# Optimization experiments

Measured on AMD Instinct MI355X. Metric: run time of the kernel, lower is better.

The kernel has to match this reference:

```python
import jax, jax.numpy as jnp
import numpy as np

S_MUL, V_MUL = 32, 16          # 32x0e + 16x1o
NODE_DIM = S_MUL + 3 * V_MUL   # 80
LATENT = 128
INV_SQRT3 = 1.0 / np.sqrt(3.0)          # wigner 3j (1,1,0) / (0,1,1) / (1,0,1) factor
C_SCALAR = np.float32(1.0 / np.sqrt(48.0))   # path_norm 'element': fan into 0e = 32*1 + 16*1
C_VECTOR = np.float32(np.sqrt(3.0 / 48.0))   # irrep dim 3 / fan 48 for 1o output


def setup_inputs() -> dict:
    rng = np.random.default_rng(0)
    B, n_atoms, radius = 2048, 32, 5.0
    N = B * n_atoms
    # atoms uniform in a 10A cube -> ~300 edges per 32-atom graph at r=5
    pos_g = rng.uniform(0.0, 10.0, size=(B, n_atoms, 3)).astype(np.float32)
    diff = pos_g[:, :, None, :] - pos_g[:, None, :, :]
    d2 = (diff * diff).sum(-1)
    mask = (d2 <= radius * radius) & (d2 > 0.0)   # same predicate as build_radius_graph
    b_idx, i_idx, j_idx = np.nonzero(mask)
    edge_index = np.stack([b_idx * n_atoms + i_idx, b_idx * n_atoms + j_idx]).astype(np.int32)
    pos = pos_g.reshape(N, 3)
    z = rng.integers(0, 100, size=N).astype(np.int32)
    batch = np.repeat(np.arange(B, dtype=np.int32), n_atoms)
    L = 3  # num_layers

    def w(*shape, scale=1.0):
        return jnp.asarray((rng.standard_normal(shape) * scale).astype(np.float32))

    return dict(
        pos=jnp.asarray(pos), z=jnp.asarray(z), batch=jnp.asarray(batch),
        edge_index=jnp.asarray(edge_index), num_graphs=B,
        emb=w(100, S_MUL),                      # nn.Embedding(100, 32) ~ N(0,1)
        W_s2n=w(S_MUL, S_MUL),                  # e3nn Linear 32x0e -> 32x0e path
        W1=w(L, S_MUL, S_MUL),                  # tp path 0e x 0e -> 0e
        W2=w(L, S_MUL, V_MUL),                  # tp path 0e x 1o -> 1o
        W3=w(L, V_MUL, V_MUL),                  # tp path 1o x 0e -> 1o
        W4=w(L, V_MUL, S_MUL),                  # tp path 1o x 1o -> 0e
        Ws=w(L, S_MUL, S_MUL),                  # e3nn Linear scalar block
        Wv=w(L, V_MUL, V_MUL),                  # e3nn Linear vector block
        Wr1=w(NODE_DIM, 256, scale=1.0 / np.sqrt(NODE_DIM)), br1=jnp.zeros((256,), jnp.float32),
        Wr2=w(256, LATENT, scale=1.0 / np.sqrt(256.0)), br2=jnp.zeros((LATENT,), jnp.float32),
    )


def _forward(pos, emb, W_s2n, W1, W2, W3, W4, Ws, Wv, Wr1, br1, Wr2, br2,
             z, batch, edge_index, num_graphs):
    N = pos.shape[0]
    src, dst = edge_index[0], edge_index[1]
    # atom embedding -> node irreps (only 0e->0e path exists; vectors start at 0)
    s = (emb[z] @ W_s2n) * np.float32(1.0 / np.sqrt(S_MUL))   # (N, 32)
    v = jnp.zeros((N, V_MUL, 3), pos.dtype)                   # (N, 16, 3)
    # spherical harmonics, normalize=True, 'component': Y0 = 1, Y1 = sqrt(3) * r_hat
    rij = pos[dst] - pos[src]                                 # (E, 3)
    sh1 = np.float32(np.sqrt(3.0)) * rij / jnp.linalg.norm(rij, axis=-1, keepdims=True)
    for l in range(W1.shape[0]):
        ss, vs = s[src], v[src]                               # gather (E,32), (E,16,3)
        # FullyConnectedTensorProduct(node, sh, node), uvw weights, sh0 == 1
        m_s = C_SCALAR * (jnp.einsum('eu,uw->ew', ss, W1[l])
                          + INV_SQRT3 * jnp.einsum('eui,ei,uw->ew', vs, sh1, W4[l]))
        m_v = (C_VECTOR * INV_SQRT3) * (jnp.einsum('eu,ei,uw->ewi', ss, sh1, W2[l])
                                        + jnp.einsum('eui,uw->ewi', vs, W3[l]))
        a_s = jax.ops.segment_sum(m_s, dst, num_segments=N)   # index_add_ scatter
        a_v = jax.ops.segment_sum(m_v, dst, num_segments=N)
        # e3nn Linear (per-irrep block, 1/sqrt(fan_in)) then relu on FULL feature (as in source)
        h_s = jax.nn.relu((a_s @ Ws[l]) * np.float32(1.0 / np.sqrt(S_MUL)))
        h_v = jax.nn.relu(jnp.einsum('nvi,vw->nwi', a_v, Wv[l]) * np.float32(1.0 / np.sqrt(V_MUL)))
        s, v = s + h_s, v + h_v                               # residual
    x = jnp.concatenate([s, v.reshape(N, V_MUL * 3)], axis=-1)  # (N, 80)
    hg = jax.ops.segment_sum(x, batch, num_segments=num_graphs) # sum-pool per graph
    return jax.nn.relu(hg @ Wr1 + br1) @ Wr2 + br2              # (B, latent)


def reference(pos, emb, W_s2n, W1, W2, W3, W4, Ws, Wv, Wr1, br1, Wr2, br2,
              z, batch, edge_index, num_graphs):
    return _forward(pos, emb, W_s2n, W1, W2, W3, W4, Ws, Wv, Wr1, br1, Wr2, br2,
                    z, batch, edge_index, num_graphs)
```

## Files before the change

kernel.cpp:

```cpp
#include <hip/hip_runtime.h>
#include <math.h>

typedef __attribute__((ext_vector_type(8))) short bf16x8;
typedef __attribute__((ext_vector_type(4))) float f32x4;

#define SQRT3F     1.7320508075688772f
#define SCALE_T    0.17677669529663687f
#define SCALE_M1   0.025515518153991442f
#define SCALE_M2   0.014731391274719739f
#define SCALE_M34  0.036084391824351615f

#define FSTR 40
#define ASTR 72

__device__ __forceinline__ ushort f2bf(float f) {
    union { float f; unsigned u; } v; v.f = f;
    unsigned u = v.u;
    return (ushort)((u + 0x7FFFu + ((u >> 16) & 1u)) >> 16);
}
__device__ __forceinline__ float bf2f(ushort h) {
    union { unsigned u; float f; } v; v.u = ((unsigned)h) << 16;
    return v.f;
}
__device__ __forceinline__ unsigned cvtpk(float lo, float hi) {
    unsigned r;
    asm("v_cvt_pk_bf16_f32 %0, %1, %2" : "=v"(r) : "v"(lo), "v"(hi));
    return r;
}
__device__ __forceinline__ f32x4 mfma(bf16x8 a, bf16x8 b, f32x4 c) {
    return __builtin_amdgcn_mfma_f32_16x16x32_bf16(a, b, c, 0, 0, 0);
}
__device__ __forceinline__ void storeAgg(ushort* AG, f32x4 t, int u0, int n) {
    uint2 u;
    u.x = cvtpk(t[0], t[1]);
    u.y = cvtpk(t[2], t[3]);
    *(uint2*)&AG[n*ASTR + u0] = u;
}
__device__ __forceinline__ void rmw4(ushort* F, int c, int n0, f32x4 h) {
    uint2* p = (uint2*)&F[c*FSTR + n0];
    uint2 o = *p;
    float f0 = bf2f((ushort)(o.x      )) + fmaxf(h[0], 0.f);
    float f1 = bf2f((ushort)(o.x >> 16)) + fmaxf(h[1], 0.f);
    float f2 = bf2f((ushort)(o.y      )) + fmaxf(h[2], 0.f);
    float f3 = bf2f((ushort)(o.y >> 16)) + fmaxf(h[3], 0.f);
    uint2 w;
    w.x = cvtpk(f0, f1);
    w.y = cvtpk(f2, f3);
    *p = w;
}

__global__ void prep_kernel(const float* __restrict__ emb,
                            const float* __restrict__ W_s2n,
                            const float* __restrict__ W1, const float* __restrict__ W2,
                            const float* __restrict__ W3, const float* __restrict__ W4,
                            const float* __restrict__ Ws, const float* __restrict__ Wv,
                            ushort* __restrict__ Tbf, ushort* __restrict__ Mbf)
{
    int idx = blockIdx.x * blockDim.x + threadIdx.x;
    if (idx < 3200) {
        int r = idx >> 5, c = idx & 31;
        float acc = 0.f;
        for (int k = 0; k < 32; ++k) acc += emb[r*32 + k] * W_s2n[k*32 + c];
        Tbf[idx] = f2bf(acc * SCALE_T);
        return;
    }
    idx -= 3200;
    if (idx < 3*48*64) {
        int lyr = idx / 3072, rem = idx % 3072;
        int row = rem >> 6, u = rem & 63;
        float val = 0.f;
        if (row < 32) {
            int w = row;
            if (u < 32) {
                float a = 0.f;
                for (int k = 0; k < 32; ++k)
                    a += W1[lyr*1024 + u*32 + k] * Ws[lyr*1024 + k*32 + w];
                val = a * SCALE_M1;
            } else if (u < 48) {
                int uu = u - 32; float a = 0.f;
                for (int k = 0; k < 32; ++k)
                    a += W4[lyr*512 + uu*32 + k] * Ws[lyr*1024 + k*32 + w];
                val = a * SCALE_M2;
            }
        } else {
            int w = row - 32;
            if (u < 32) {
                float a = 0.f;
                for (int k = 0; k < 16; ++k)
                    a += W2[lyr*512 + u*16 + k] * Wv[lyr*256 + k*16 + w];
                val = a * SCALE_M34;
            } else if (u < 48) {
                int uu = u - 32; float a = 0.f;
                for (int k = 0; k < 16; ++k)
                    a += W3[lyr*256 + uu*16 + k] * Wv[lyr*256 + k*16 + w];
                val = a * SCALE_M34;
            }
        }
        Mbf[lyr*3072 + row*64 + u] = f2bf(val);
    }
}

__global__ __launch_bounds__(256)
void gnn_kernel(const float* __restrict__ pos, const int* __restrict__ z,
                const ushort* __restrict__ Tbf, const ushort* __restrict__ Mbf,
                const float* __restrict__ Wr1, const float* __restrict__ br1,
                const float* __restrict__ Wr2, const float* __restrict__ br2,
                float* __restrict__ out, int B)
{
    __shared__ __align__(16) char smem[45312];
    ushort* featA = (ushort*)smem;
    ushort* aggA  = (ushort*)(smem + 25600);
    float*  hgl   = (float*)(smem + 44032);
    float*  h1    = (float*)aggA;
    float*  red   = ((float*)aggA) + 1024;

    const int tid = threadIdx.x;
    const int wv = tid >> 6, l = tid & 63;
    const int g  = blockIdx.x*4 + wv;
    ushort* F  = featA + wv*80*FSTR;
    ushort* AG = aggA  + wv*32*ASTR;

    for (int i = l; i < 32*(ASTR/2); i += 64) ((uint*)AG)[i] = 0;
    for (int i = l; i < 48*(FSTR/2); i += 64) ((uint*)(F + 32*FSTR))[i] = 0;

    {
        int n = l & 31, h = l >> 5;
        int zg = z[g*32 + n];
        uint4 t0 = *(const uint4*)(Tbf + zg*32 + h*16);
        uint4 t1 = *(const uint4*)(Tbf + zg*32 + h*16 + 8);
        unsigned ua[8] = {t0.x, t0.y, t0.z, t0.w, t1.x, t1.y, t1.z, t1.w};
        #pragma unroll
        for (int q = 0; q < 8; ++q) {
            F[(h*16 + 2*q    )*FSTR + n] = (ushort)ua[q];
            F[(h*16 + 2*q + 1)*FSTR + n] = (ushort)(ua[q] >> 16);
        }
    }

    const int ln = l & 15, kq = l >> 4;
    bf16x8 adjf[4][2];
    {
        const int k0 = kq*8;
        #pragma unroll
        for (int nt = 0; nt < 2; ++nt) {
            int ng = g*32 + nt*16 + ln;
            float px = pos[3*ng], py = pos[3*ng+1], pz = pos[3*ng+2];
            union { bf16x8 v; ushort s[8]; } o[4];
            #pragma unroll
            for (int jj = 0; jj < 8; ++jj) {
                int j = g*32 + k0 + jj;
                float dx = __fsub_rn(px, pos[3*j]);
                float dy = __fsub_rn(py, pos[3*j+1]);
                float dz = __fsub_rn(pz, pos[3*j+2]);
                float d2 = __fadd_rn(__fadd_rn(__fmul_rn(dx,dx), __fmul_rn(dy,dy)),
                                     __fmul_rn(dz,dz));
                bool on = (d2 <= 25.0f) && (d2 > 0.0f);
                float rinv = on ? rsqrtf(d2) * SQRT3F : 0.f;
                o[0].s[jj] = on ? (ushort)0x3F80 : (ushort)0;
                o[1].s[jj] = f2bf(dx * rinv);
                o[2].s[jj] = f2bf(dy * rinv);
                o[3].s[jj] = f2bf(dz * rinv);
            }
            #pragma unroll
            for (int w = 0; w < 4; ++w) adjf[w][nt] = o[w].v;
        }
    }

    const f32x4 z4 = {0.f, 0.f, 0.f, 0.f};

    for (int lay = 0; lay < 3; ++lay) {
        const ushort* Mg = Mbf + lay*3072;
        bf16x8 fs0 = *(const bf16x8*)&F[(     ln)*FSTR + kq*8];
        bf16x8 fs1 = *(const bf16x8*)&F[(16 + ln)*FSTR + kq*8];
        bf16x8 fv0 = *(const bf16x8*)&F[(32 + ln)*FSTR + kq*8];
        bf16x8 fv1 = *(const bf16x8*)&F[(48 + ln)*FSTR + kq*8];
        bf16x8 fv2 = *(const bf16x8*)&F[(64 + ln)*FSTR + kq*8];
        bf16x8 bmS0[2], bmS1[2], bmV[2];
        #pragma unroll
        for (int kc = 0; kc < 2; ++kc) {
            bmS0[kc] = *(const bf16x8*)&Mg[(     ln)*64 + kc*32 + kq*8];
            bmS1[kc] = *(const bf16x8*)&Mg[(16 + ln)*64 + kc*32 + kq*8];
            bmV [kc] = *(const bf16x8*)&Mg[(32 + ln)*64 + kc*32 + kq*8];
        }

        #pragma unroll
        for (int nt = 0; nt < 2; ++nt) {
            f32x4 t;
            t = mfma(fs0, adjf[0][nt], z4);
            storeAgg(AG, t,      kq*4, nt*16 + ln);
            t = mfma(fs1, adjf[0][nt], z4);
            storeAgg(AG, t, 16 + kq*4, nt*16 + ln);
            t = mfma(fv2, adjf[3][nt], z4);
            t = mfma(fv1, adjf[2][nt], t);
            t = mfma(fv0, adjf[1][nt], t);
            storeAgg(AG, t, 32 + kq*4, nt*16 + ln);
        }
        f32x4 hs[2][2] = {{z4, z4}, {z4, z4}};
        #pragma unroll
        for (int kc = 0; kc < 2; ++kc)
            #pragma unroll
            for (int mt = 0; mt < 2; ++mt) {
                bf16x8 ag = *(const bf16x8*)&AG[(mt*16 + ln)*ASTR + kc*32 + kq*8];
                hs[mt][0] = mfma(ag, bmS0[kc], hs[mt][0]);
                hs[mt][1] = mfma(ag, bmS1[kc], hs[mt][1]);
            }
        #pragma unroll
        for (int mt = 0; mt < 2; ++mt)
            #pragma unroll
            for (int wt = 0; wt < 2; ++wt)
                rmw4(F, wt*16 + ln, mt*16 + kq*4, hs[mt][wt]);

        #pragma unroll
        for (int i = 0; i < 3; ++i) {
            bf16x8 fvi = (i == 0) ? fv0 : (i == 1) ? fv1 : fv2;
            #pragma unroll
            for (int nt = 0; nt < 2; ++nt) {
                f32x4 t;
                t = mfma(fs0, adjf[1+i][nt], z4);
                storeAgg(AG, t,      kq*4, nt*16 + ln);
                t = mfma(fs1, adjf[1+i][nt], z4);
                storeAgg(AG, t, 16 + kq*4, nt*16 + ln);
                t = mfma(fvi, adjf[0][nt], z4);
                storeAgg(AG, t, 32 + kq*4, nt*16 + ln);
            }
            f32x4 hv[2] = {z4, z4};
            #pragma unroll
            for (int kc = 0; kc < 2; ++kc)
                #pragma unroll
                for (int mt = 0; mt < 2; ++mt) {
                    bf16x8 ag = *(const bf16x8*)&AG[(mt*16 + ln)*ASTR + kc*32 + kq*8];
                    hv[mt] = mfma(ag, bmV[kc], hv[mt]);
                }
            #pragma unroll
            for (int mt = 0; mt < 2; ++mt)
                rmw4(F, 32 + i*16 + ln, mt*16 + kq*4, hv[mt]);
        }
    }

    for (int f = l; f < 80; f += 64) {
        const ushort* row;
        if (f < 32) row = &F[f*FSTR];
        else { int c = f - 32, w = c/3, i = c - 3*w; row = &F[(32 + i*16 + w)*FSTR]; }
        const uint* r32 = (const uint*)row;
        float acc = 0.f;
        #pragma unroll
        for (int q = 0; q < 16; ++q) {
            uint u = r32[q];
            acc += bf2f((ushort)u) + bf2f((ushort)(u >> 16));
        }
        hgl[wv*80 + f] = acc;
    }
    __syncthreads();

    {
        const int w = tid;
        float acc0 = br1[w];
        float acc1 = acc0, acc2 = acc0, acc3 = acc0;
        #pragma unroll 4
        for (int f = 0; f < 80; ++f) {
            float wvv = Wr1[f*256 + w];
            acc0 = fmaf(hgl[0*80 + f], wvv, acc0);
            acc1 = fmaf(hgl[1*80 + f], wvv, acc1);
            acc2 = fmaf(hgl[2*80 + f], wvv, acc2);
            acc3 = fmaf(hgl[3*80 + f], wvv, acc3);
        }
        h1[0*256 + w] = fmaxf(acc0, 0.f);
        h1[1*256 + w] = fmaxf(acc1, 0.f);
        h1[2*256 + w] = fmaxf(acc2, 0.f);
        h1[3*256 + w] = fmaxf(acc3, 0.f);
    }
    __syncthreads();
    {
        const int g0 = blockIdx.x * 4;
        const int w2 = tid & 127, kh = tid >> 7;
        const float4* h1v = (const float4*)h1;
        float s0 = 0.f, s1 = 0.f, s2 = 0.f, s3 = 0.f;
        #pragma unroll 2
        for (int k4 = kh*32; k4 < kh*32 + 32; ++k4) {
            float4 hA = h1v[0*64 + k4];
            float4 hB = h1v[1*64 + k4];
            float4 hC = h1v[2*64 + k4];
            float4 hD = h1v[3*64 + k4];
            int k = k4 * 4;
            float m0 = Wr2[(size_t)(k+0)*128 + w2];
            float m1 = Wr2[(size_t)(k+1)*128 + w2];
            float m2 = Wr2[(size_t)(k+2)*128 + w2];
            float m3 = Wr2[(size_t)(k+3)*128 + w2];
            s0 = fmaf(hA.x,m0, fmaf(hA.y,m1, fmaf(hA.z,m2, fmaf(hA.w,m3, s0))));
            s1 = fmaf(hB.x,m0, fmaf(hB.y,m1, fmaf(hB.z,m2, fmaf(hB.w,m3, s1))));
            s2 = fmaf(hC.x,m0, fmaf(hC.y,m1, fmaf(hC.z,m2, fmaf(hC.w,m3, s2))));
            s3 = fmaf(hD.x,m0, fmaf(hD.y,m1, fmaf(hD.z,m2, fmaf(hD.w,m3, s3))));
        }
        if (kh) {
            red[0*128 + w2] = s0; red[1*128 + w2] = s1;
            red[2*128 + w2] = s2; red[3*128 + w2] = s3;
        }
        __syncthreads();
        if (!kh) {
            float b = br2[w2];
            out[(size_t)(g0+0)*128 + w2] = s0 + red[0*128 + w2] + b;
            out[(size_t)(g0+1)*128 + w2] = s1 + red[1*128 + w2] + b;
            out[(size_t)(g0+2)*128 + w2] = s2 + red[2*128 + w2] + b;
            out[(size_t)(g0+3)*128 + w2] = s3 + red[3*128 + w2] + b;
        }
    }
}

extern "C" void kernel_launch(void* const* d_in, const int* in_sizes, int n_in,
                              void* d_out, int out_size, void* d_ws, size_t ws_size,
                              hipStream_t stream)
{
    const float* pos   = (const float*)d_in[0];
    const int*   z     = (const int*)d_in[1];
    const float* emb   = (const float*)d_in[5];
    const float* W_s2n = (const float*)d_in[6];
    const float* W1    = (const float*)d_in[7];
    const float* W2    = (const float*)d_in[8];
    const float* W3    = (const float*)d_in[9];
    const float* W4    = (const float*)d_in[10];
    const float* Ws    = (const float*)d_in[11];
    const float* Wv    = (const float*)d_in[12];
    const float* Wr1   = (const float*)d_in[13];
    const float* br1   = (const float*)d_in[14];
    const float* Wr2   = (const float*)d_in[15];
    const float* br2   = (const float*)d_in[16];
    float* out = (float*)d_out;

    const int B = out_size / 128;

    char* p = (char*)d_ws;
    ushort* Tbf = (ushort*)p;  p += 6400;
    ushort* Mbf = (ushort*)p;  p += 18432;

    const int prep_total = 3200 + 3*48*64;
    prep_kernel<<<(prep_total + 255) / 256, 256, 0, stream>>>(
        emb, W_s2n, W1, W2, W3, W4, Ws, Wv, Tbf, Mbf);

    gnn_kernel<<<B / 4, 256, 0, stream>>>(pos, z, Tbf, Mbf,
                                          Wr1, br1, Wr2, br2, out, B);
}
```

Before: 113.8 us.

## Keep aggregation tiles in registers via permlane swaps instead of LDS

The aggregated MFMA outputs are now repacked directly into B-operand fragments with permlane32/permlane16 swaps, instead of being written to a shared-memory staging buffer and reloaded. This drops the LDS store/load round trip and cuts shared memory per block, which may allow more blocks per CU. In exchange it adds software bf16 rounding and cross-lane permute instructions, and the register-to-fragment layout has to be exactly right.

```diff
diff --git a/kernel.cpp b/kernel.cpp
--- a/kernel.cpp
+++ b/kernel.cpp
@@ -11,7 +11,6 @@
 #define SCALE_M34  0.036084391824351615f
 
 #define FSTR 40
-#define ASTR 72
 
 __device__ __forceinline__ ushort f2bf(float f) {
     union { float f; unsigned u; } v; v.f = f;
@@ -22,19 +21,38 @@
     union { unsigned u; float f; } v; v.u = ((unsigned)h) << 16;
     return v.f;
 }
+__device__ __forceinline__ unsigned packbf(float lo, float hi) {
+    return (unsigned)f2bf(lo) | ((unsigned)f2bf(hi) << 16);
+}
 __device__ __forceinline__ unsigned cvtpk(float lo, float hi) {
     unsigned r;
     asm("v_cvt_pk_bf16_f32 %0, %1, %2" : "=v"(r) : "v"(lo), "v"(hi));
     return r;
 }
+__device__ __forceinline__ void pl32(unsigned &a, unsigned &b) {
+    auto r = __builtin_amdgcn_permlane32_swap(a, b, false, false);
+    a = r[0]; b = r[1];
+}
+__device__ __forceinline__ void pl16(unsigned &a, unsigned &b) {
+    auto r = __builtin_amdgcn_permlane16_swap(a, b, false, false);
+    a = r[0]; b = r[1];
+}
 __device__ __forceinline__ f32x4 mfma(bf16x8 a, bf16x8 b, f32x4 c) {
     return __builtin_amdgcn_mfma_f32_16x16x32_bf16(a, b, c, 0, 0, 0);
 }
-__device__ __forceinline__ void storeAgg(ushort* AG, f32x4 t, int u0, int n) {
-    uint2 u;
-    u.x = cvtpk(t[0], t[1]);
-    u.y = cvtpk(t[2], t[3]);
-    *(uint2*)&AG[n*ASTR + u0] = u;
+__device__ __forceinline__ void makeFrags(f32x4 T0, f32x4 T1, f32x4 T2,
+                                          bf16x8 &f0, bf16x8 &f1) {
+    unsigned p0 = packbf(T0[0], T0[1]), p1 = packbf(T0[2], T0[3]);
+    unsigned q0 = packbf(T1[0], T1[1]), q1 = packbf(T1[2], T1[3]);
+    unsigned s0 = packbf(T2[0], T2[1]), s1 = packbf(T2[2], T2[3]);
+    pl32(p0, q0); pl16(p0, q0);
+    pl32(p1, q1); pl16(p1, q1);
+    unsigned z0 = 0u, z1 = 0u;
+    pl32(s0, z0); pl16(s0, z0);
+    pl32(s1, z1); pl16(s1, z1);
+    union { bf16x8 v; unsigned u[4]; } r;
+    r.u[0] = p0; r.u[1] = p1; r.u[2] = q0; r.u[3] = q1; f0 = r.v;
+    r.u[0] = s0; r.u[1] = s1; r.u[2] = z0; r.u[3] = z1; f1 = r.v;
 }
 __device__ __forceinline__ void rmw4(ushort* F, int c, int n0, f32x4 h) {
     uint2* p = (uint2*)&F[c*FSTR + n0];
@@ -107,20 +125,17 @@
                 const float* __restrict__ Wr2, const float* __restrict__ br2,
                 float* __restrict__ out, int B)
 {
-    __shared__ __align__(16) char smem[45312];
+    __shared__ __align__(16) char smem[26880];
     ushort* featA = (ushort*)smem;
-    ushort* aggA  = (ushort*)(smem + 25600);
-    float*  hgl   = (float*)(smem + 44032);
-    float*  h1    = (float*)aggA;
-    float*  red   = ((float*)aggA) + 1024;
+    float*  hgl   = (float*)(smem + 25600);
+    float*  h1    = (float*)smem;
+    float*  red   = (float*)(smem + 4096);
 
     const int tid = threadIdx.x;
     const int wv = tid >> 6, l = tid & 63;
     const int g  = blockIdx.x*4 + wv;
     ushort* F  = featA + wv*80*FSTR;
-    ushort* AG = aggA  + wv*32*ASTR;
-
-    for (int i = l; i < 32*(ASTR/2); i += 64) ((uint*)AG)[i] = 0;
+
     for (int i = l; i < 48*(FSTR/2); i += 64) ((uint*)(F + 32*FSTR))[i] = 0;
 
     {
@@ -182,26 +197,24 @@
             bmV [kc] = *(const bf16x8*)&Mg[(32 + ln)*64 + kc*32 + kq*8];
         }
 
+        bf16x8 agf[2][2];
+
         #pragma unroll
         for (int nt = 0; nt < 2; ++nt) {
-            f32x4 t;
-            t = mfma(fs0, adjf[0][nt], z4);
-            storeAgg(AG, t,      kq*4, nt*16 + ln);
-            t = mfma(fs1, adjf[0][nt], z4);
-            storeAgg(AG, t, 16 + kq*4, nt*16 + ln);
-            t = mfma(fv2, adjf[3][nt], z4);
-            t = mfma(fv1, adjf[2][nt], t);
-            t = mfma(fv0, adjf[1][nt], t);
-            storeAgg(AG, t, 32 + kq*4, nt*16 + ln);
+            f32x4 T0 = mfma(fs0, adjf[0][nt], z4);
+            f32x4 T1 = mfma(fs1, adjf[0][nt], z4);
+            f32x4 T2 = mfma(fv2, adjf[3][nt], z4);
+            T2 = mfma(fv1, adjf[2][nt], T2);
+            T2 = mfma(fv0, adjf[1][nt], T2);
+            makeFrags(T0, T1, T2, agf[nt][0], agf[nt][1]);
         }
         f32x4 hs[2][2] = {{z4, z4}, {z4, z4}};
         #pragma unroll
         for (int kc = 0; kc < 2; ++kc)
             #pragma unroll
             for (int mt = 0; mt < 2; ++mt) {
-                bf16x8 ag = *(const bf16x8*)&AG[(mt*16 + ln)*ASTR + kc*32 + kq*8];
-                hs[mt][0] = mfma(ag, bmS0[kc], hs[mt][0]);
-                hs[mt][1] = mfma(ag, bmS1[kc], hs[mt][1]);
+                hs[mt][0] = mfma(agf[mt][kc], bmS0[kc], hs[mt][0]);
+                hs[mt][1] = mfma(agf[mt][kc], bmS1[kc], hs[mt][1]);
             }
         #pragma unroll
         for (int mt = 0; mt < 2; ++mt)
@@ -214,22 +227,17 @@
             bf16x8 fvi = (i == 0) ? fv0 : (i == 1) ? fv1 : fv2;
             #pragma unroll
             for (int nt = 0; nt < 2; ++nt) {
-                f32x4 t;
-                t = mfma(fs0, adjf[1+i][nt], z4);
-                storeAgg(AG, t,      kq*4, nt*16 + ln);
-                t = mfma(fs1, adjf[1+i][nt], z4);
-                storeAgg(AG, t, 16 + kq*4, nt*16 + ln);
-                t = mfma(fvi, adjf[0][nt], z4);
-                storeAgg(AG, t, 32 + kq*4, nt*16 + ln);
+                f32x4 T0 = mfma(fs0, adjf[1+i][nt], z4);
+                f32x4 T1 = mfma(fs1, adjf[1+i][nt], z4);
+                f32x4 T2 = mfma(fvi, adjf[0][nt], z4);
+                makeFrags(T0, T1, T2, agf[nt][0], agf[nt][1]);
             }
             f32x4 hv[2] = {z4, z4};
             #pragma unroll
             for (int kc = 0; kc < 2; ++kc)
                 #pragma unroll
-                for (int mt = 0; mt < 2; ++mt) {
-                    bf16x8 ag = *(const bf16x8*)&AG[(mt*16 + ln)*ASTR + kc*32 + kq*8];
-                    hv[mt] = mfma(ag, bmV[kc], hv[mt]);
-                }
+                for (int mt = 0; mt < 2; ++mt)
+                    hv[mt] = mfma(agf[mt][kc], bmV[kc], hv[mt]);
             #pragma unroll
             for (int mt = 0; mt < 2; ++mt)
                 rmw4(F, 32 + i*16 + ln, mt*16 + kq*4, hv[mt]);
```

Result: no change. 112.8 us (-0.9%).
